# Optimization experiments

Measured on AMD Instinct MI355X. Metric: run time of the kernel, lower is better.

The kernel has to match this reference:

```python
import jax, jax.numpy as jnp
import numpy as np

B, J, FIN, FOUT = 8192, 17, 128, 128
BN_EPS = 1e-5


def setup_inputs() -> dict:
    key = jax.random.key(0)
    k_x, k_w, k_adj, k_b = jax.random.split(key, 4)
    x = jax.random.normal(k_x, (B, J, FIN), dtype=jnp.float32)
    # Xavier-uniform-ish init for W [2, FIN, FOUT]
    limit = 1.414 * np.sqrt(6.0 / (FIN + FOUT))
    W = jax.random.uniform(k_w, (2, FIN, FOUT), minval=-limit, maxval=limit, dtype=jnp.float32)
    M = jnp.ones((J, FOUT), dtype=jnp.float32)
    # binary-ish skeleton adjacency buffer (constant)
    adj = (jax.random.uniform(k_adj, (J, J)) > 0.7).astype(jnp.float32)
    adj = adj + jnp.eye(J, dtype=jnp.float32)  # self loops like skeleton graphs
    adj2 = jnp.full((J, J), 1e-6, dtype=jnp.float32)
    stdv = 1.0 / np.sqrt(FOUT)
    bias = jax.random.uniform(k_b, (FOUT,), minval=-stdv, maxval=stdv, dtype=jnp.float32)
    gamma = jnp.ones((FOUT,), dtype=jnp.float32)
    beta = jnp.zeros((FOUT,), dtype=jnp.float32)
    return {"x": x, "W": W, "M": M, "adj": adj, "adj2": adj2,
            "bias": bias, "gamma": gamma, "beta": beta}


def reference(x, W, M, adj, adj2, bias, gamma, beta):
    # ModulatedGraphConv
    h0 = jnp.einsum('bjf,fo->bjo', x, W[0])
    h1 = jnp.einsum('bjf,fo->bjo', x, W[1])
    a = adj + adj2
    a = (a.T + a) * 0.5                       # symmetrize [J, J]
    diag = jnp.diagonal(a)                    # [J]
    off = a * (1.0 - jnp.eye(a.shape[0], dtype=a.dtype))  # zero diagonal
    # diag part: adj*E is diagonal -> per-node scaling; off-diag: dense matmul over J
    out = diag[None, :, None] * (M * h0) + jnp.einsum('ij,bjo->bio', off, M * h1)
    out = out + bias[None, None, :]           # [B, J, FOUT]
    # BatchNorm1d over channel dim (training-mode batch stats over B and J)
    mean = out.mean(axis=(0, 1))
    var = out.var(axis=(0, 1))                # biased variance, as torch BN uses
    out = (out - mean) * jax.lax.rsqrt(var + BN_EPS) * gamma + beta
    return jax.nn.relu(out)
```

## Files before the change

### kernel.cpp

```cpp
#include <hip/hip_runtime.h>


#define NSLOT 64
#define OFF_PART   0
#define OFF_STATS  16384
#define OFF_OFFSYM 16640
#define OFF_DIAG   16929
#define OFF_WBT    16960

typedef __attribute__((ext_vector_type(8))) short bf16x8;
typedef __attribute__((ext_vector_type(4))) short bf16x4;
typedef __attribute__((ext_vector_type(4))) float f32x4;

__device__ __forceinline__ short f2bf(float f) {
    unsigned u = __float_as_uint(f);
    u += 0x7FFFu + ((u >> 16) & 1u);
    return (short)(u >> 16);
}
__device__ __forceinline__ float bf2f(short h) {
    return __uint_as_float(((unsigned)(unsigned short)h) << 16);
}

__global__ __launch_bounds__(256) void prep_kernel(
    const float* __restrict__ W, const float* __restrict__ adj,
    const float* __restrict__ adj2, float* __restrict__ wsf)
{
    const int t = threadIdx.x;
    short* wbt = (short*)(wsf + OFF_WBT);
    const int sel = t >> 7, np = t & 127;
    const float* wsrc = W + sel * 16384 + np;
    #pragma unroll 8
    for (int k = 0; k < 128; ++k)
        wbt[t * 128 + k] = f2bf(wsrc[k * 128]);
    for (int e = t; e < 289; e += 256) {
        int i = e / 17, j = e % 17;
        float v = 0.5f * (adj[i*17+j] + adj2[i*17+j] + adj[j*17+i] + adj2[j*17+i]);
        if (i == j) { wsf[OFF_DIAG + i] = v; v = 0.f; }
        wsf[OFF_OFFSYM + i*17 + j] = v;
    }
}

__global__ __launch_bounds__(512, 4) void conv_kernel(
    const float* __restrict__ x, const float* __restrict__ M,
    const float* __restrict__ bias, float* __restrict__ out,
    float* __restrict__ wsf)
{
    __shared__ short A_lds[80][136];
    __shared__ short hh[68][260];
    __shared__ float red[512], red2[512];

    const int tid = threadIdx.x;
    const int w = tid >> 6, l = tid & 63, c = l & 15, g = l >> 4;

    const float4* xsrc = (const float4*)(x + (size_t)blockIdx.x * (68 * 128));
    #pragma unroll
    for (int it = 0; it < 5; ++it) {
        int f = tid + it * 512;
        if (f < 2176) {
            float4 v = xsrc[f];
            int r = f >> 5, k0 = (f & 31) << 2;
            bf16x4 p;
            p[0] = f2bf(v.x); p[1] = f2bf(v.y); p[2] = f2bf(v.z); p[3] = f2bf(v.w);
            *(bf16x4*)&A_lds[r][k0] = p;
        }
    }
    if (tid < 408) {
        bf16x4 z = {0, 0, 0, 0};
        ((bf16x4*)&A_lds[68][0])[tid] = z;
    }
    __syncthreads();

    const short* wbt = (const short*)(wsf + OFF_WBT);
    const int cb = w * 32;
    f32x4 acc[5][2];
    #pragma unroll
    for (int mt = 0; mt < 5; ++mt)
        #pragma unroll
        for (int nt = 0; nt < 2; ++nt)
            acc[mt][nt] = (f32x4){0.f, 0.f, 0.f, 0.f};

    #pragma unroll
    for (int ks = 0; ks < 4; ++ks) {
        bf16x8 bf0 = *(const bf16x8*)(wbt + (cb + c) * 128      + ks * 32 + g * 8);
        bf16x8 bf1 = *(const bf16x8*)(wbt + (cb + 16 + c) * 128 + ks * 32 + g * 8);
        #pragma unroll
        for (int mt = 0; mt < 5; ++mt) {
            bf16x8 af = *(const bf16x8*)&A_lds[mt * 16 + c][ks * 32 + g * 8];
            acc[mt][0] = __builtin_amdgcn_mfma_f32_16x16x32_bf16(af, bf0, acc[mt][0], 0, 0, 0);
            acc[mt][1] = __builtin_amdgcn_mfma_f32_16x16x32_bf16(af, bf1, acc[mt][1], 0, 0, 0);
        }
    }

    #pragma unroll
    for (int mt = 0; mt < 5; ++mt) {
        int row0 = mt * 16 + g * 4;
        #pragma unroll
        for (int nt = 0; nt < 2; ++nt) {
            #pragma unroll
            for (int r = 0; r < 4; ++r) {
                int row = row0 + r;
                if (row < 68) hh[row][cb + nt * 16 + c] = f2bf(acc[mt][nt][r]);
            }
        }
    }
    __syncthreads();

    const int bb = tid >> 7;
    const int o  = tid & 127;
    const float* offp  = wsf + OFF_OFFSYM;
    const float* diagp = wsf + OFF_DIAG;
    const int rbase = bb * 17;
    const float bv = bias[o];

    float vout[17];
    #pragma unroll
    for (int i = 0; i < 17; ++i) {
        float h0v = bf2f(hh[rbase + i][o]);
        vout[i] = fmaf(diagp[i] * M[i * 128 + o], h0v, bv);
    }
    #pragma unroll
    for (int j = 0; j < 17; ++j) {
        float h1v = bf2f(hh[rbase + j][128 + o]) * M[j * 128 + o];
        #pragma unroll
        for (int i = 0; i < 17; ++i)
            vout[i] = fmaf(offp[i * 17 + j], h1v, vout[i]);
    }

    float s = 0.f, s2 = 0.f;
    float* op = out + ((size_t)blockIdx.x * 68 + rbase) * 128 + o;
    #pragma unroll
    for (int i = 0; i < 17; ++i) {
        float v = vout[i];
        op[i * 128] = v;
        s += v; s2 = fmaf(v, v, s2);
    }

    red[tid] = s; red2[tid] = s2;
    __syncthreads();
    if (tid < 128) {
        float ts = red[tid] + red[tid + 128] + red[tid + 256] + red[tid + 384];
        float t2 = red2[tid] + red2[tid + 128] + red2[tid + 256] + red2[tid + 384];
        float* slot = wsf + OFF_PART + ((blockIdx.x & (NSLOT - 1)) << 8);
        atomicAdd(slot + tid, ts);
        atomicAdd(slot + 128 + tid, t2);
    }
}

__global__ __launch_bounds__(256) void bn_reduce_kernel(
    const float* __restrict__ part, const float* __restrict__ gamma,
    const float* __restrict__ beta, float* __restrict__ stats)
{
    const int t = threadIdx.x;
    float s = 0.f;
    #pragma unroll 8
    for (int i = 0; i < NSLOT; ++i) s += part[i * 256 + t];
    __shared__ float tot[256];
    tot[t] = s;
    __syncthreads();
    if (t < 128) {
        const float n = 139264.f;
        float mean = tot[t] / n;
        float var  = tot[t + 128] / n - mean * mean;
        var = fmaxf(var, 0.f);
        float inv = rsqrtf(var + 1e-5f);
        float sc = gamma[t] * inv;
        stats[t] = sc;
        stats[t + 128] = beta[t] - mean * sc;
    }
}

__global__ __launch_bounds__(256) void apply_kernel(
    float* __restrict__ out, const float* __restrict__ stats, int n4)
{
    const int tid = blockIdx.x * 256 + threadIdx.x;
    const int c0 = (tid << 2) & 127;
    const float sc0 = stats[c0],     sc1 = stats[c0 + 1],
                sc2 = stats[c0 + 2], sc3 = stats[c0 + 3];
    const float sh0 = stats[128 + c0],     sh1 = stats[128 + c0 + 1],
                sh2 = stats[128 + c0 + 2], sh3 = stats[128 + c0 + 3];
    float4* o4 = (float4*)out;
    for (int q = tid; q < n4; q += 2048 * 256) {
        float4 v = o4[q];
        v.x = fmaxf(fmaf(v.x, sc0, sh0), 0.f);
        v.y = fmaxf(fmaf(v.y, sc1, sh1), 0.f);
        v.z = fmaxf(fmaf(v.z, sc2, sh2), 0.f);
        v.w = fmaxf(fmaf(v.w, sc3, sh3), 0.f);
        o4[q] = v;
    }
}

extern "C" void kernel_launch(void* const* d_in, const int* in_sizes, int n_in,
                              void* d_out, int out_size, void* d_ws, size_t ws_size,
                              hipStream_t stream) {
    (void)in_sizes; (void)n_in; (void)out_size; (void)ws_size;
    const float* x     = (const float*)d_in[0];
    const float* W     = (const float*)d_in[1];
    const float* M     = (const float*)d_in[2];
    const float* adj   = (const float*)d_in[3];
    const float* adj2  = (const float*)d_in[4];
    const float* bias  = (const float*)d_in[5];
    const float* gamma = (const float*)d_in[6];
    const float* beta  = (const float*)d_in[7];
    float* out = (float*)d_out;
    float* wsf = (float*)d_ws;

    hipMemsetAsync(d_ws, 0, NSLOT * 256 * sizeof(float), stream);
    prep_kernel<<<1, 256, 0, stream>>>(W, adj, adj2, wsf);
    conv_kernel<<<2048, 512, 0, stream>>>(x, M, bias, out, wsf);
    bn_reduce_kernel<<<1, 256, 0, stream>>>(wsf + OFF_PART, gamma, beta, wsf + OFF_STATS);
    apply_kernel<<<2048, 256, 0, stream>>>(out, wsf + OFF_STATS, 4456448);
}
```

Before: 87.35 us.

## Store pre-BN activations as bf16 in workspace and halve conv block size

The conv kernel now handles 34 rows per block with 4096 blocks and a smaller LDS footprint, aiming for higher occupancy. It folds the diag, M and bias scaling into the MFMA epilogue and packs h0/h1 as bf16 pairs. When the workspace is large enough, it writes pre-BN values as bf16 to scratch, and a new apply kernel reads bf16 and writes fp32, cutting intermediate traffic. The extra bf16 rounding of pre-BN values adds precision risk, and the atomic slots are doubled.

New measurement: 97.40 us. 1.12x slower.

```diff
diff --git a/kernel.cpp b/kernel.cpp
--- a/kernel.cpp
+++ b/kernel.cpp
@@ -1,12 +1,14 @@
 #include <hip/hip_runtime.h>
 
 
-#define NSLOT 64
+#define NSLOT      128
 #define OFF_PART   0
-#define OFF_STATS  16384
-#define OFF_OFFSYM 16640
-#define OFF_DIAG   16929
-#define OFF_WBT    16960
+#define OFF_STATS  32768
+#define OFF_OFFSYM 33024
+#define OFF_DIAG   33313
+#define OFF_WBT    33344
+#define OFF_PRE    49728
+#define PRE_SHORTS (139264ull * 128ull)
 
 typedef __attribute__((ext_vector_type(8))) short bf16x8;
 typedef __attribute__((ext_vector_type(4))) short bf16x4;
@@ -19,6 +21,12 @@
 }
 __device__ __forceinline__ float bf2f(short h) {
     return __uint_as_float(((unsigned)(unsigned short)h) << 16);
+}
+__device__ __forceinline__ float bflo(int p) {
+    return __uint_as_float(((unsigned)p) << 16);
+}
+__device__ __forceinline__ float bfhi(int p) {
+    return __uint_as_float(((unsigned)p) & 0xFFFF0000u);
 }
 
 __global__ __launch_bounds__(256) void prep_kernel(
@@ -40,107 +48,136 @@
     }
 }
 
-__global__ __launch_bounds__(512, 4) void conv_kernel(
+template<int USE_BF16>
+__global__ __launch_bounds__(512, 8) void conv_kernel(
     const float* __restrict__ x, const float* __restrict__ M,
-    const float* __restrict__ bias, float* __restrict__ out,
-    float* __restrict__ wsf)
-{
-    __shared__ short A_lds[80][136];
-    __shared__ short hh[68][260];
-    __shared__ float red[512], red2[512];
+    const float* __restrict__ bias, float* ws,
+    float* __restrict__ out, short* __restrict__ pre)
+{
+    __shared__ int U[34 * 140];
+    __shared__ float offs[292];
+    short (*A)[136] = (short(*)[136])U;
+    int* hhI = U;
 
     const int tid = threadIdx.x;
     const int w = tid >> 6, l = tid & 63, c = l & 15, g = l >> 4;
 
-    const float4* xsrc = (const float4*)(x + (size_t)blockIdx.x * (68 * 128));
-    #pragma unroll
-    for (int it = 0; it < 5; ++it) {
+    for (int e = tid; e < 289; e += 512) offs[e] = ws[OFF_OFFSYM + e];
+
+    const float4* xsrc = (const float4*)(x + (size_t)blockIdx.x * (34 * 128));
+    #pragma unroll
+    for (int it = 0; it < 3; ++it) {
         int f = tid + it * 512;
-        if (f < 2176) {
+        if (f < 1088) {
             float4 v = xsrc[f];
             int r = f >> 5, k0 = (f & 31) << 2;
             bf16x4 p;
             p[0] = f2bf(v.x); p[1] = f2bf(v.y); p[2] = f2bf(v.z); p[3] = f2bf(v.w);
-            *(bf16x4*)&A_lds[r][k0] = p;
-        }
-    }
-    if (tid < 408) {
+            *(bf16x4*)&A[r][k0] = p;
+        }
+    }
+    if (tid < 476) {
         bf16x4 z = {0, 0, 0, 0};
-        ((bf16x4*)&A_lds[68][0])[tid] = z;
-    }
-    __syncthreads();
-
-    const short* wbt = (const short*)(wsf + OFF_WBT);
-    const int cb = w * 32;
-    f32x4 acc[5][2];
-    #pragma unroll
-    for (int mt = 0; mt < 5; ++mt)
-        #pragma unroll
-        for (int nt = 0; nt < 2; ++nt)
-            acc[mt][nt] = (f32x4){0.f, 0.f, 0.f, 0.f};
-
+        ((bf16x4*)&A[34][0])[tid] = z;
+    }
+    __syncthreads();
+
+    const short* wbt = (const short*)(ws + OFF_WBT);
+    const int col = w * 16 + c;
+    f32x4 acc0[3], acc1[3];
+    #pragma unroll
+    for (int mt = 0; mt < 3; ++mt) {
+        acc0[mt] = (f32x4){0.f, 0.f, 0.f, 0.f};
+        acc1[mt] = (f32x4){0.f, 0.f, 0.f, 0.f};
+    }
     #pragma unroll
     for (int ks = 0; ks < 4; ++ks) {
-        bf16x8 bf0 = *(const bf16x8*)(wbt + (cb + c) * 128      + ks * 32 + g * 8);
-        bf16x8 bf1 = *(const bf16x8*)(wbt + (cb + 16 + c) * 128 + ks * 32 + g * 8);
-        #pragma unroll
-        for (int mt = 0; mt < 5; ++mt) {
-            bf16x8 af = *(const bf16x8*)&A_lds[mt * 16 + c][ks * 32 + g * 8];
-            acc[mt][0] = __builtin_amdgcn_mfma_f32_16x16x32_bf16(af, bf0, acc[mt][0], 0, 0, 0);
-            acc[mt][1] = __builtin_amdgcn_mfma_f32_16x16x32_bf16(af, bf1, acc[mt][1], 0, 0, 0);
-        }
-    }
-
-    #pragma unroll
-    for (int mt = 0; mt < 5; ++mt) {
-        int row0 = mt * 16 + g * 4;
-        #pragma unroll
-        for (int nt = 0; nt < 2; ++nt) {
+        bf16x8 b0 = *(const bf16x8*)(wbt + col * 128 + ks * 32 + g * 8);
+        bf16x8 b1 = *(const bf16x8*)(wbt + (col + 128) * 128 + ks * 32 + g * 8);
+        #pragma unroll
+        for (int mt = 0; mt < 3; ++mt) {
+            bf16x8 af = *(const bf16x8*)&A[mt * 16 + c][ks * 32 + g * 8];
+            acc0[mt] = __builtin_amdgcn_mfma_f32_16x16x32_bf16(af, b0, acc0[mt], 0, 0, 0);
+            acc1[mt] = __builtin_amdgcn_mfma_f32_16x16x32_bf16(af, b1, acc1[mt], 0, 0, 0);
+        }
+    }
+    __syncthreads();
+
+    const float bv = bias[col];
+    #pragma unroll
+    for (int mt = 0; mt < 3; ++mt) {
+        #pragma unroll
+        for (int r = 0; r < 4; ++r) {
+            int row = mt * 16 + g * 4 + r;
+            if (row < 34) {
+                int j = row - 17 * ((row * 241) >> 12);
+                float m  = M[j * 128 + col];
+                float dg = ws[OFF_DIAG + j];
+                float lo = fmaf(dg * m, acc0[mt][r], bv);
+                float hi = m * acc1[mt][r];
+                unsigned pk = ((unsigned)(unsigned short)f2bf(lo)) |
+                              (((unsigned)(unsigned short)f2bf(hi)) << 16);
+                hhI[row * 140 + col] = (int)pk;
+            }
+        }
+    }
+    __syncthreads();
+
+    const int half = tid >> 8, bb = (tid >> 7) & 1, o = tid & 127;
+    const int rb = bb * 17;
+    int pj[17];
+    #pragma unroll
+    for (int i = 0; i < 17; ++i) pj[i] = hhI[(rb + i) * 140 + o];
+    __syncthreads();
+
+    float s = 0.f, s2 = 0.f;
+    const size_t gbase = ((size_t)blockIdx.x * 34 + rb) * 128 + o;
+    if (half == 0) {
+        float vout[9];
+        #pragma unroll
+        for (int q = 0; q < 9; ++q) vout[q] = bflo(pj[q]);
+        #pragma unroll
+        for (int j = 0; j < 17; ++j) {
+            float h1v = bfhi(pj[j]);
             #pragma unroll
-            for (int r = 0; r < 4; ++r) {
-                int row = row0 + r;
-                if (row < 68) hh[row][cb + nt * 16 + c] = f2bf(acc[mt][nt][r]);
-            }
-        }
-    }
-    __syncthreads();
-
-    const int bb = tid >> 7;
-    const int o  = tid & 127;
-    const float* offp  = wsf + OFF_OFFSYM;
-    const float* diagp = wsf + OFF_DIAG;
-    const int rbase = bb * 17;
-    const float bv = bias[o];
-
-    float vout[17];
-    #pragma unroll
-    for (int i = 0; i < 17; ++i) {
-        float h0v = bf2f(hh[rbase + i][o]);
-        vout[i] = fmaf(diagp[i] * M[i * 128 + o], h0v, bv);
-    }
-    #pragma unroll
-    for (int j = 0; j < 17; ++j) {
-        float h1v = bf2f(hh[rbase + j][128 + o]) * M[j * 128 + o];
-        #pragma unroll
-        for (int i = 0; i < 17; ++i)
-            vout[i] = fmaf(offp[i * 17 + j], h1v, vout[i]);
-    }
-
-    float s = 0.f, s2 = 0.f;
-    float* op = out + ((size_t)blockIdx.x * 68 + rbase) * 128 + o;
-    #pragma unroll
-    for (int i = 0; i < 17; ++i) {
-        float v = vout[i];
-        op[i * 128] = v;
-        s += v; s2 = fmaf(v, v, s2);
-    }
-
-    red[tid] = s; red2[tid] = s2;
+            for (int q = 0; q < 9; ++q)
+                vout[q] = fmaf(offs[q * 17 + j], h1v, vout[q]);
+        }
+        #pragma unroll
+        for (int q = 0; q < 9; ++q) {
+            float v = vout[q];
+            if (USE_BF16) pre[gbase + (size_t)q * 128] = f2bf(v);
+            else          out[gbase + (size_t)q * 128] = v;
+            s += v; s2 = fmaf(v, v, s2);
+        }
+    } else {
+        float vout[8];
+        #pragma unroll
+        for (int q = 0; q < 8; ++q) vout[q] = bflo(pj[9 + q]);
+        #pragma unroll
+        for (int j = 0; j < 17; ++j) {
+            float h1v = bfhi(pj[j]);
+            #pragma unroll
+            for (int q = 0; q < 8; ++q)
+                vout[q] = fmaf(offs[(9 + q) * 17 + j], h1v, vout[q]);
+        }
+        #pragma unroll
+        for (int q = 0; q < 8; ++q) {
+            float v = vout[q];
+            if (USE_BF16) pre[gbase + (size_t)(9 + q) * 128] = f2bf(v);
+            else          out[gbase + (size_t)(9 + q) * 128] = v;
+            s += v; s2 = fmaf(v, v, s2);
+        }
+    }
+
+    float* red = (float*)U;
+    red[tid] = s; red[512 + tid] = s2;
     __syncthreads();
     if (tid < 128) {
         float ts = red[tid] + red[tid + 128] + red[tid + 256] + red[tid + 384];
-        float t2 = red2[tid] + red2[tid + 128] + red2[tid + 256] + red2[tid + 384];
-        float* slot = wsf + OFF_PART + ((blockIdx.x & (NSLOT - 1)) << 8);
+        float t2 = red[512 + tid] + red[512 + tid + 128] +
+                   red[512 + tid + 256] + red[512 + tid + 384];
+        float* slot = ws + OFF_PART + ((blockIdx.x & (NSLOT - 1)) << 8);
         atomicAdd(slot + tid, ts);
         atomicAdd(slot + 128 + tid, t2);
     }
@@ -166,6 +203,32 @@
         float sc = gamma[t] * inv;
         stats[t] = sc;
         stats[t + 128] = beta[t] - mean * sc;
+    }
+}
+
+__global__ __launch_bounds__(256) void apply_bf16_kernel(
+    const short* __restrict__ pre, const float* __restrict__ stats,
+    float* __restrict__ out)
+{
+    const int tid = blockIdx.x * 256 + threadIdx.x;
+    const int c0 = (tid << 3) & 127;
+    float sc[8], sh[8];
+    #pragma unroll
+    for (int e = 0; e < 8; ++e) { sc[e] = stats[c0 + e]; sh[e] = stats[128 + c0 + e]; }
+    const bf16x8* p8 = (const bf16x8*)pre;
+    for (int q = tid; q < 2228224; q += 524288) {
+        bf16x8 v = p8[q];
+        float4 o0, o1;
+        o0.x = fmaxf(fmaf(bf2f(v[0]), sc[0], sh[0]), 0.f);
+        o0.y = fmaxf(fmaf(bf2f(v[1]), sc[1], sh[1]), 0.f);
+        o0.z = fmaxf(fmaf(bf2f(v[2]), sc[2], sh[2]), 0.f);
+        o0.w = fmaxf(fmaf(bf2f(v[3]), sc[3], sh[3]), 0.f);
+        o1.x = fmaxf(fmaf(bf2f(v[4]), sc[4], sh[4]), 0.f);
+        o1.y = fmaxf(fmaf(bf2f(v[5]), sc[5], sh[5]), 0.f);
+        o1.z = fmaxf(fmaf(bf2f(v[6]), sc[6], sh[6]), 0.f);
+        o1.w = fmaxf(fmaf(bf2f(v[7]), sc[7], sh[7]), 0.f);
+        float4* dst = (float4*)(out + (size_t)q * 8);
+        dst[0] = o0; dst[1] = o1;
     }
 }
 
@@ -192,7 +255,7 @@
 extern "C" void kernel_launch(void* const* d_in, const int* in_sizes, int n_in,
                               void* d_out, int out_size, void* d_ws, size_t ws_size,
                               hipStream_t stream) {
-    (void)in_sizes; (void)n_in; (void)out_size; (void)ws_size;
+    (void)in_sizes; (void)n_in; (void)out_size;
     const float* x     = (const float*)d_in[0];
     const float* W     = (const float*)d_in[1];
     const float* M     = (const float*)d_in[2];
@@ -203,10 +266,19 @@
     const float* beta  = (const float*)d_in[7];
     float* out = (float*)d_out;
     float* wsf = (float*)d_ws;
+    short* pre = (short*)(wsf + OFF_PRE);
+
+    const bool big = ws_size >= (size_t)OFF_PRE * 4 + PRE_SHORTS * 2;
 
     hipMemsetAsync(d_ws, 0, NSLOT * 256 * sizeof(float), stream);
     prep_kernel<<<1, 256, 0, stream>>>(W, adj, adj2, wsf);
-    conv_kernel<<<2048, 512, 0, stream>>>(x, M, bias, out, wsf);
-    bn_reduce_kernel<<<1, 256, 0, stream>>>(wsf + OFF_PART, gamma, beta, wsf + OFF_STATS);
-    apply_kernel<<<2048, 256, 0, stream>>>(out, wsf + OFF_STATS, 4456448);
-}
+    if (big) {
+        conv_kernel<1><<<4096, 512, 0, stream>>>(x, M, bias, wsf, out, pre);
+        bn_reduce_kernel<<<1, 256, 0, stream>>>(wsf + OFF_PART, gamma, beta, wsf + OFF_STATS);
+        apply_bf16_kernel<<<2048, 256, 0, stream>>>(pre, wsf + OFF_STATS, out);
+    } else {
+        conv_kernel<0><<<4096, 512, 0, stream>>>(x, M, bias, wsf, out, pre);
+        bn_reduce_kernel<<<1, 256, 0, stream>>>(wsf + OFF_PART, gamma, beta, wsf + OFF_STATS);
+        apply_kernel<<<2048, 256, 0, stream>>>(out, wsf + OFF_STATS, 4456448);
+    }
+}
```
